# Performance work log

Measured on AMD Instinct MI355X. Metric: run time of the kernel, lower is better.

Reference implementation:

```python
import jax, jax.numpy as jnp
import numpy as np

B, NF, IN = 8, 4096, 512
NB, NW, CD = 2, 320, 384  # num_codebooks, num_codewords, codeword_dim (d_model=NB*CD=768)
TAU = 1.0


def setup_inputs() -> dict:
    key = jax.random.key(0)
    k0, k1, k2, k3, k4 = jax.random.split(key, 5)
    x = jax.random.normal(k0, (B, NF, IN), dtype=jnp.float32)
    mask = jax.random.randint(k1, (B, NF), 0, 2) == 1  # True = invalid frame
    u = jax.random.uniform(k2, (B, NF, NB, NW), jnp.float32, 1e-6, 1.0 - 1e-6)
    gumbel = -jnp.log(-jnp.log(u))
    # projection Linear(IN -> NB*NW)
    W = jax.random.normal(k3, (IN, NB * NW), jnp.float32) * np.float32(1.0 / np.sqrt(IN))
    b = jnp.zeros((NB * NW,), jnp.float32)
    # codebooks, xavier-uniform-ish init
    limit = np.float32(np.sqrt(6.0 / (NW + CD)))
    codebooks = jax.random.uniform(k4, (NB, NW, CD), jnp.float32, -limit, limit)
    return dict(x=x, W=W, b=b, codebooks=codebooks, gumbel=gumbel, mask=mask)


def reference(x, W, b, codebooks, gumbel, mask):
    Bx, NFx = x.shape[:2]
    logits = (x @ W + b).reshape(Bx, NFx, NB, NW)  # (b, nf, nb, nw)
    # hard gumbel-softmax with straight-through estimator (training path)
    y = (logits + gumbel) / TAU
    soft = jax.nn.softmax(y, axis=-1)
    hard = jax.nn.one_hot(jnp.argmax(y, axis=-1), NW, dtype=soft.dtype)
    word_probs = hard + soft - jax.lax.stop_gradient(soft)
    # diversity perplexity from plain softmax probs, masked; note: faithful to
    # source, normalization divides by mask.sum() (count of invalid frames)
    soft_probs = jax.nn.softmax(logits, axis=-1)
    valid = (~mask)[..., None, None].astype(soft_probs.dtype)
    marginal = jnp.sum(soft_probs * valid, axis=(0, 1)) / mask.sum().astype(soft_probs.dtype)
    perplexity = jnp.exp(-jnp.sum(marginal * jnp.log(marginal + 1e-7), axis=-1)).sum()
    # quantize: one-hot gather-sum over codewords, concat codebooks -> d_model
    quantized = jnp.einsum('bfnw,nwd->bfnd', word_probs, codebooks).reshape(Bx, NFx, NB * CD)
    return quantized, perplexity
```

## Files before the change

kernel.cpp:

```cpp
#include <hip/hip_runtime.h>
#include <math.h>

#define BQ   8
#define NFQ  4096
#define INQ  512
#define NBQ  2
#define NWQ  320
#define CDQ  384
#define MQ   (BQ*NFQ)
#define NTOT (NBQ*NWQ)
#define DMOD (NBQ*CDQ)
#define QOUT ((size_t)MQ*(size_t)DMOD)

#define THREADS 512
#define BM 64
#define BK 32
#define NCH (INQ/BK)
#define NMB (MQ/BM)

#define A0B 0
#define A1B 4096
#define B0B 8192
#define B1B 28672
#define SMEMB 49152
#define SSUMB 8192
#define AYMB  9216
#define AIDXB 10240
#define SCB   11264
#define IDXB  11520
#define CALB  11776

#define WT_OFF   0
#define PART_OFF 655360
#define CS_OFF   1310720
#define MC_OFF   1313280

typedef __attribute__((ext_vector_type(4))) float f32x4;
typedef __attribute__((ext_vector_type(8))) short short8;
typedef const __attribute__((address_space(1))) unsigned short gas_us;
typedef __attribute__((address_space(3))) unsigned short las_us;

static __device__ __forceinline__ unsigned f2bf(float f) {
    unsigned u = __float_as_uint(f);
    return (u + 0x7FFFu + ((u >> 16) & 1u)) >> 16;
}

static __device__ __forceinline__ uint4 pack8u(float4 a, float4 b) {
    return make_uint4(f2bf(a.x) | (f2bf(a.y) << 16),
                      f2bf(a.z) | (f2bf(a.w) << 16),
                      f2bf(b.x) | (f2bf(b.y) << 16),
                      f2bf(b.z) | (f2bf(b.w) << 16));
}

#define MCOL(M,N) \
  acc##M##N = __builtin_amdgcn_mfma_f32_16x16x32_bf16(fa##M, fb##N, acc##M##N,0,0,0);

#define STAGE_B(KC, BASE) do { \
  const unsigned short* wp_ = WtB + (KC)*BK; \
  __builtin_amdgcn_global_load_lds((gas_us*)(wp_ + gb0), (las_us*)(smem + (BASE) + lo0), 16, 0, 0); \
  __builtin_amdgcn_global_load_lds((gas_us*)(wp_ + gb1), (las_us*)(smem + (BASE) + lo1), 16, 0, 0); \
  if (tid < 256) \
    __builtin_amdgcn_global_load_lds((gas_us*)(wp_ + gb2), (las_us*)(smem + (BASE) + lo2), 16, 0, 0); \
} while(0)

#define EPI1(M,R) do { \
  const int row_ = rh*32 + M*16 + q*4 + (R); \
  const int gm_  = m0 + row_; \
  float s_ = __expf(acc##M##0[R]) + __expf(acc##M##1[R]) + __expf(acc##M##2[R]) \
           + __expf(acc##M##3[R]) + __expf(acc##M##4[R]); \
  s_ += __shfl_xor(s_,1,64); s_ += __shfl_xor(s_,2,64); \
  s_ += __shfl_xor(s_,4,64); s_ += __shfl_xor(s_,8,64); \
  const float* gp_ = gum + (size_t)gm_*NTOT + nb*NWQ + cg*80 + c15; \
  float ym_ = acc##M##0[R] + gp_[0]; int yi_ = c15; float yt_; \
  yt_ = acc##M##1[R] + gp_[16]; if (yt_>ym_){ym_=yt_; yi_=16+c15;} \
  yt_ = acc##M##2[R] + gp_[32]; if (yt_>ym_){ym_=yt_; yi_=32+c15;} \
  yt_ = acc##M##3[R] + gp_[48]; if (yt_>ym_){ym_=yt_; yi_=48+c15;} \
  yt_ = acc##M##4[R] + gp_[64]; if (yt_>ym_){ym_=yt_; yi_=64+c15;} \
  yi_ += cg*80; \
  { float ov_; int oi_; \
    ov_=__shfl_xor(ym_,1,64); oi_=__shfl_xor(yi_,1,64); if(ov_>ym_||(ov_==ym_&&oi_<yi_)){ym_=ov_;yi_=oi_;} \
    ov_=__shfl_xor(ym_,2,64); oi_=__shfl_xor(yi_,2,64); if(ov_>ym_||(ov_==ym_&&oi_<yi_)){ym_=ov_;yi_=oi_;} \
    ov_=__shfl_xor(ym_,4,64); oi_=__shfl_xor(yi_,4,64); if(ov_>ym_||(ov_==ym_&&oi_<yi_)){ym_=ov_;yi_=oi_;} \
    ov_=__shfl_xor(ym_,8,64); oi_=__shfl_xor(yi_,8,64); if(ov_>ym_||(ov_==ym_&&oi_<yi_)){ym_=ov_;yi_=oi_;} } \
  if (c15 == 0) { \
    ((float*)(smem+SSUMB))[cg*64 + row_] = s_; \
    ((float*)(smem+AYMB ))[cg*64 + row_] = ym_; \
    ((int*  )(smem+AIDXB))[cg*64 + row_] = yi_; } \
} while(0)

#define EPI2(M,R) do { \
  const int row_ = rh*32 + M*16 + q*4 + (R); \
  const float sc_ = ((float*)(smem+SCB))[row_]; \
  ca0 = fmaf(__expf(acc##M##0[R]), sc_, ca0); \
  ca1 = fmaf(__expf(acc##M##1[R]), sc_, ca1); \
  ca2 = fmaf(__expf(acc##M##2[R]), sc_, ca2); \
  ca3 = fmaf(__expf(acc##M##3[R]), sc_, ca3); \
  ca4 = fmaf(__expf(acc##M##4[R]), sc_, ca4); \
} while(0)

__global__ __launch_bounds__(256) void wcvt(const float* __restrict__ W,
                                            unsigned short* __restrict__ Wt)
{
    __shared__ __align__(16) float sm[64][68];
    const int kb = blockIdx.x, cbk = blockIdx.y;
    const int tid = threadIdx.x;
    const int r = tid >> 2, qq = tid & 3;
    const float* wp = W + (size_t)(kb*64 + r)*NTOT + cbk*64;
    *(float4*)(&sm[r][(qq   )*4]) = *(const float4*)(wp + (qq   )*4);
    *(float4*)(&sm[r][(qq+ 4)*4]) = *(const float4*)(wp + (qq+ 4)*4);
    *(float4*)(&sm[r][(qq+ 8)*4]) = *(const float4*)(wp + (qq+ 8)*4);
    *(float4*)(&sm[r][(qq+12)*4]) = *(const float4*)(wp + (qq+12)*4);
    __syncthreads();
    const int cc = tid >> 2, kq = tid & 3;
    const int k0 = kq * 16;
    const float v0=sm[k0+0][cc],  v1=sm[k0+1][cc],  v2=sm[k0+2][cc],  v3=sm[k0+3][cc],
                v4=sm[k0+4][cc],  v5=sm[k0+5][cc],  v6=sm[k0+6][cc],  v7=sm[k0+7][cc],
                v8=sm[k0+8][cc],  v9=sm[k0+9][cc],  v10=sm[k0+10][cc],v11=sm[k0+11][cc],
                v12=sm[k0+12][cc],v13=sm[k0+13][cc],v14=sm[k0+14][cc],v15=sm[k0+15][cc];
    const unsigned u0 = f2bf(v0)  | (f2bf(v1) <<16), u1 = f2bf(v2)  | (f2bf(v3) <<16),
                   u2 = f2bf(v4)  | (f2bf(v5) <<16), u3 = f2bf(v6)  | (f2bf(v7) <<16),
                   u4 = f2bf(v8)  | (f2bf(v9) <<16), u5 = f2bf(v10) | (f2bf(v11)<<16),
                   u6 = f2bf(v12) | (f2bf(v13)<<16), u7 = f2bf(v14) | (f2bf(v15)<<16);
    unsigned short* op = Wt + (size_t)(cbk*64 + cc)*INQ + kb*64 + k0;
    *(uint4*)(op)     = make_uint4(u0,u1,u2,u3);
    *(uint4*)(op + 8) = make_uint4(u4,u5,u6,u7);
}

__global__ __launch_bounds__(THREADS, 4) void qk1(
    const float* __restrict__ x, const unsigned short* __restrict__ Wt,
    const float* __restrict__ bias, const float* __restrict__ cb,
    const float* __restrict__ gum, const int* __restrict__ maskp,
    float* __restrict__ out, unsigned short* __restrict__ partial)
{
    __shared__ __align__(16) char smem[SMEMB];
    const int tid = threadIdx.x;
    const int orig = blockIdx.x;
    const int bid = ((orig & 7) << 7) | (orig >> 3);
    const int mb = bid >> 1, nb = bid & 1;
    const int m0 = mb * BM;
    const int w = tid >> 6, l = tid & 63, q = l >> 4, c15 = l & 15;
    const int cg = w & 3, rh = w >> 2;

    const int sB = tid & 3;
    const int colj0 = (tid      ) >> 2, colj1 = (tid +  512) >> 2,
              colj2 = (tid + 1024) >> 2;
    const int kgj0 = sB ^ ((colj0 >> 1) & 3), kgj1 = sB ^ ((colj1 >> 1) & 3),
              kgj2 = sB ^ ((colj2 >> 1) & 3);
    const unsigned short* WtB = Wt + (size_t)nb * NWQ * INQ;
    const int gb0 = colj0*INQ + kgj0*8, gb1 = colj1*INQ + kgj1*8,
              gb2 = colj2*INQ + kgj2*8;
    const int lo0 = (tid      )*16, lo1 = (tid+ 512)*16, lo2 = (tid+1024)*16;

    const int xt = tid & 255;
    const int xrow = xt >> 2, xh = xt & 3;
    const float* xg = x + (size_t)(m0 + xrow)*INQ + xh*8;
    const int axw = xrow*64 + ((xh ^ ((xrow >> 1) & 3)) * 16);

    const int sw = (c15 >> 1) & 3;
    const int aoff = (rh*32 + c15)*64 + ((q ^ sw) * 16);
    const int boff = (cg*80 + c15)*64 + ((q ^ sw) * 16);

    f32x4 acc00={0,0,0,0}, acc01={0,0,0,0}, acc02={0,0,0,0}, acc03={0,0,0,0}, acc04={0,0,0,0};
    f32x4 acc10={0,0,0,0}, acc11={0,0,0,0}, acc12={0,0,0,0}, acc13={0,0,0,0}, acc14={0,0,0,0};

    STAGE_B(0, B0B);
    if (tid < 256) {
        const float4 a0 = *(const float4*)(xg), a1 = *(const float4*)(xg + 4);
        *(uint4*)(smem + A0B + axw) = pack8u(a0, a1);
    }
    __syncthreads();

#pragma unroll 2
    for (int kc = 0; kc < NCH; ++kc) {
        const int p = kc & 1;
        const int Acur = p ? A1B : A0B;
        const int Anx  = p ? A0B : A1B;
        const int Bcur = p ? B1B : B0B;
        const int Bnx  = p ? B0B : B1B;
        const bool more = (kc + 1 < NCH);
        float4 n0, n1;
        if (more) {
            if (tid < 256) {
                n0 = *(const float4*)(xg + (kc+1)*BK);
                n1 = *(const float4*)(xg + (kc+1)*BK + 4);
            }
            STAGE_B(kc + 1, Bnx);
        }
        const short8 fa0 = *(const short8*)(smem + Acur + aoff);
        const short8 fa1 = *(const short8*)(smem + Acur + aoff + 1024);
        const short8 fb0 = *(const short8*)(smem + Bcur + boff);
        const short8 fb1 = *(const short8*)(smem + Bcur + boff + 1024);
        const short8 fb2 = *(const short8*)(smem + Bcur + boff + 2048);
        const short8 fb3 = *(const short8*)(smem + Bcur + boff + 3072);
        const short8 fb4 = *(const short8*)(smem + Bcur + boff + 4096);
        MCOL(0,0); MCOL(0,1); MCOL(0,2); MCOL(0,3); MCOL(0,4);
        MCOL(1,0); MCOL(1,1); MCOL(1,2); MCOL(1,3); MCOL(1,4);
        if (more && tid < 256)
            *(uint4*)(smem + Anx + axw) = pack8u(n0, n1);
        __syncthreads();
    }

    const float* bp = bias + nb*NWQ + cg*80 + c15;
    const float b0v = bp[0], b1v = bp[16], b2v = bp[32], b3v = bp[48], b4v = bp[64];
    acc00 = acc00 + b0v; acc01 = acc01 + b1v; acc02 = acc02 + b2v;
    acc03 = acc03 + b3v; acc04 = acc04 + b4v;
    acc10 = acc10 + b0v; acc11 = acc11 + b1v; acc12 = acc12 + b2v;
    acc13 = acc13 + b3v; acc14 = acc14 + b4v;

    EPI1(0,0); EPI1(0,1); EPI1(0,2); EPI1(0,3);
    EPI1(1,0); EPI1(1,1); EPI1(1,2); EPI1(1,3);
    __syncthreads();

    if (tid < BM) {
        const int row = tid;
        const float* ssum = (const float*)(smem + SSUMB);
        const float* aym  = (const float*)(smem + AYMB);
        const int*   aidx = (const int*)(smem + AIDXB);
        const float se = ssum[row] + ssum[64+row] + ssum[128+row] + ssum[192+row];
        const float vf = (maskp[m0 + row] == 0) ? 1.0f : 0.0f;
        ((float*)(smem + SCB))[row] = vf / se;
        float bv = aym[row]; int bi = aidx[row];
        float ov; int oi;
        ov = aym[ 64+row]; oi = aidx[ 64+row]; if (ov>bv || (ov==bv && oi<bi)) { bv=ov; bi=oi; }
        ov = aym[128+row]; oi = aidx[128+row]; if (ov>bv || (ov==bv && oi<bi)) { bv=ov; bi=oi; }
        ov = aym[192+row]; oi = aidx[192+row]; if (ov>bv || (ov==bv && oi<bi)) { bv=ov; bi=oi; }
        ((int*)(smem + IDXB))[row] = bi;
    }
    __syncthreads();

    float ca0=0.f, ca1=0.f, ca2=0.f, ca3=0.f, ca4=0.f;
    EPI2(0,0); EPI2(0,1); EPI2(0,2); EPI2(0,3);
    EPI2(1,0); EPI2(1,1); EPI2(1,2); EPI2(1,3);
    ca0 += __shfl_xor(ca0,16,64); ca0 += __shfl_xor(ca0,32,64);
    ca1 += __shfl_xor(ca1,16,64); ca1 += __shfl_xor(ca1,32,64);
    ca2 += __shfl_xor(ca2,16,64); ca2 += __shfl_xor(ca2,32,64);
    ca3 += __shfl_xor(ca3,16,64); ca3 += __shfl_xor(ca3,32,64);
    ca4 += __shfl_xor(ca4,16,64); ca4 += __shfl_xor(ca4,32,64);
    if (l < 16) {
        float* cal = (float*)(smem + CALB) + w*80 + c15;
        cal[0]=ca0; cal[16]=ca1; cal[32]=ca2; cal[48]=ca3; cal[64]=ca4;
    }
    __syncthreads();
    if (tid < NWQ) {
        const float* cal = (const float*)(smem + CALB);
        const float v = cal[tid] + cal[tid + 320];
        partial[(size_t)mb*NTOT + nb*NWQ + tid] = (unsigned short)f2bf(v);
    }

    const float* cbb = cb + (size_t)nb*NWQ*CDQ;
    const int* idxs = (const int*)(smem + IDXB);
    for (int t = tid; t < BM*(CDQ/4); t += THREADS) {
        const int r = t / (CDQ/4);
        const int qq = t - r*(CDQ/4);
        const int idx = idxs[r];
        float4 v = *(const float4*)(cbb + (size_t)idx*CDQ + qq*4);
        *(float4*)(out + (size_t)(m0+r)*DMOD + (size_t)nb*CDQ + qq*4) = v;
    }
}

__global__ __launch_bounds__(256) void qk2a(const unsigned short* __restrict__ partial,
                                            const int* __restrict__ maskp,
                                            float* __restrict__ colsum,
                                            int* __restrict__ maskcnt)
{
    __shared__ float fs[256];
    __shared__ int   is[4];
    const int b = blockIdx.x, tid = threadIdx.x;
    if (b < 40) {
        const int ci = tid & 15, g = tid >> 4;
        const int col = b*16 + ci;
        float s = 0.f;
        for (int r = 0; r < 32; ++r) {
            const unsigned u = partial[(size_t)(g*32 + r)*NTOT + col];
            s += __uint_as_float(u << 16);
        }
        fs[g*16 + ci] = s;
        __syncthreads();
        if (tid < 16) {
            float t = 0.f;
            for (int g2 = 0; g2 < 16; ++g2) t += fs[g2*16 + tid];
            colsum[b*16 + tid] = t;
        }
    } else {
        const int bb = b - 40;
        int ms = 0;
        for (int k2 = 0; k2 < 16; ++k2) ms += maskp[bb*4096 + tid + k2*256];
        for (int s2 = 32; s2 >= 1; s2 >>= 1) ms += __shfl_xor(ms, s2, 64);
        if ((tid & 63) == 0) is[tid >> 6] = ms;
        __syncthreads();
        if (tid == 0) maskcnt[bb] = is[0] + is[1] + is[2] + is[3];
    }
}

__global__ void qk2b(const float* __restrict__ colsum,
                     const int* __restrict__ maskcnt,
                     float* __restrict__ out)
{
    __shared__ float fred[10];
    __shared__ float s_ms;
    const int tid = threadIdx.x, lane = tid & 63, wid = tid >> 6;
    if (tid == 0) {
        int t = 0;
        for (int i = 0; i < 8; ++i) t += maskcnt[i];
        s_ms = (float)t;
    }
    __syncthreads();
    float mar = colsum[tid] / s_ms;
    float tv = mar * logf(mar + 1e-7f);
    for (int s = 32; s >= 1; s >>= 1) tv += __shfl_xor(tv, s, 64);
    if (lane == 0) fred[wid] = tv;
    __syncthreads();
    if (tid == 0) {
        float h0 = fred[0]+fred[1]+fred[2]+fred[3]+fred[4];
        float h1 = fred[5]+fred[6]+fred[7]+fred[8]+fred[9];
        out[QOUT] = expf(-h0) + expf(-h1);
    }
}

extern "C" void kernel_launch(void* const* d_in, const int* in_sizes, int n_in,
                              void* d_out, int out_size, void* d_ws, size_t ws_size,
                              hipStream_t stream) {
    const float* x    = (const float*)d_in[0];
    const float* W    = (const float*)d_in[1];
    const float* bias = (const float*)d_in[2];
    const float* cb   = (const float*)d_in[3];
    const float* gum  = (const float*)d_in[4];
    const int*   mask = (const int*)d_in[5];
    float* out = (float*)d_out;
    unsigned short* Wt      = (unsigned short*)((char*)d_ws + WT_OFF);
    unsigned short* partial = (unsigned short*)((char*)d_ws + PART_OFF);
    float*          colsum  = (float*)((char*)d_ws + CS_OFF);
    int*            maskcnt = (int*)((char*)d_ws + MC_OFF);

    wcvt<<<dim3(INQ/64, NTOT/64), 256, 0, stream>>>(W, Wt);
    qk1<<<NMB*NBQ, THREADS, 0, stream>>>(x, Wt, bias, cb, gum, mask, out, partial);
    qk2a<<<48, 256, 0, stream>>>(partial, mask, colsum, maskcnt);
    qk2b<<<1, 640, 0, stream>>>(colsum, maskcnt, out);
}
```

Baseline: 81.41 us.

## Fuse perplexity finalize into reduction kernel via last-block atomic; drop block swizzle

Merges the two final reduction kernels into one: each of the 48 blocks increments an atomic counter after a threadfence, and the last block computes the entropy and perplexity. This removes one kernel launch and its dependency gap. The counter is reset inside the weight-conversion kernel. It also removes the blockIdx remapping in the main fused kernel, which changes block scheduling order and L2 locality for the x tiles.

```diff
diff --git a/kernel.cpp b/kernel.cpp
--- a/kernel.cpp
+++ b/kernel.cpp
@@ -34,6 +34,7 @@
 #define PART_OFF 655360
 #define CS_OFF   1310720
 #define MC_OFF   1313280
+#define CNT_OFF  1313312
 
 typedef __attribute__((ext_vector_type(4))) float f32x4;
 typedef __attribute__((ext_vector_type(8))) short short8;
@@ -99,11 +100,13 @@
 } while(0)
 
 __global__ __launch_bounds__(256) void wcvt(const float* __restrict__ W,
-                                            unsigned short* __restrict__ Wt)
+                                            unsigned short* __restrict__ Wt,
+                                            int* __restrict__ cnt)
 {
     __shared__ __align__(16) float sm[64][68];
     const int kb = blockIdx.x, cbk = blockIdx.y;
     const int tid = threadIdx.x;
+    if (kb == 0 && cbk == 0 && tid == 0) *cnt = 0;
     const int r = tid >> 2, qq = tid & 3;
     const float* wp = W + (size_t)(kb*64 + r)*NTOT + cbk*64;
     *(float4*)(&sm[r][(qq   )*4]) = *(const float4*)(wp + (qq   )*4);
@@ -134,8 +137,7 @@
 {
     __shared__ __align__(16) char smem[SMEMB];
     const int tid = threadIdx.x;
-    const int orig = blockIdx.x;
-    const int bid = ((orig & 7) << 7) | (orig >> 3);
+    const int bid = blockIdx.x;
     const int mb = bid >> 1, nb = bid & 1;
     const int m0 = mb * BM;
     const int w = tid >> 6, l = tid & 63, q = l >> 4, c15 = l & 15;
@@ -258,13 +260,16 @@
     }
 }
 
-__global__ __launch_bounds__(256) void qk2a(const unsigned short* __restrict__ partial,
-                                            const int* __restrict__ maskp,
-                                            float* __restrict__ colsum,
-                                            int* __restrict__ maskcnt)
+__global__ __launch_bounds__(256) void qk2(const unsigned short* __restrict__ partial,
+                                           const int* __restrict__ maskp,
+                                           float* __restrict__ colsum,
+                                           int* __restrict__ maskcnt,
+                                           int* __restrict__ cnt,
+                                           float* __restrict__ out)
 {
     __shared__ float fs[256];
     __shared__ int   is[4];
+    __shared__ int   lastf;
     const int b = blockIdx.x, tid = threadIdx.x;
     if (b < 40) {
         const int ci = tid & 15, g = tid >> 4;
@@ -290,30 +295,39 @@
         __syncthreads();
         if (tid == 0) maskcnt[bb] = is[0] + is[1] + is[2] + is[3];
     }
-}
-
-__global__ void qk2b(const float* __restrict__ colsum,
-                     const int* __restrict__ maskcnt,
-                     float* __restrict__ out)
-{
-    __shared__ float fred[10];
-    __shared__ float s_ms;
-    const int tid = threadIdx.x, lane = tid & 63, wid = tid >> 6;
+    __threadfence();
+    if (tid == 0) {
+        const int old = atomicAdd(cnt, 1);
+        lastf = (old == 47);
+    }
+    __syncthreads();
+    if (!lastf) return;
+    __threadfence();
+
     if (tid == 0) {
         int t = 0;
         for (int i = 0; i < 8; ++i) t += maskcnt[i];
-        s_ms = (float)t;
-    }
-    __syncthreads();
-    float mar = colsum[tid] / s_ms;
-    float tv = mar * logf(mar + 1e-7f);
-    for (int s = 32; s >= 1; s >>= 1) tv += __shfl_xor(tv, s, 64);
-    if (lane == 0) fred[wid] = tv;
+        fs[0] = (float)t;
+    }
+    __syncthreads();
+    const float sm_f = fs[0];
+    float h0 = 0.f, h1 = 0.f;
+    for (int c = tid; c < NTOT; c += 256) {
+        const float mar = colsum[c] / sm_f;
+        const float tv = mar * logf(mar + 1e-7f);
+        if (c < NWQ) h0 += tv; else h1 += tv;
+    }
+    for (int s2 = 32; s2 >= 1; s2 >>= 1) {
+        h0 += __shfl_xor(h0, s2, 64);
+        h1 += __shfl_xor(h1, s2, 64);
+    }
+    __syncthreads();
+    if ((tid & 63) == 0) { fs[tid >> 6] = h0; fs[4 + (tid >> 6)] = h1; }
     __syncthreads();
     if (tid == 0) {
-        float h0 = fred[0]+fred[1]+fred[2]+fred[3]+fred[4];
-        float h1 = fred[5]+fred[6]+fred[7]+fred[8]+fred[9];
-        out[QOUT] = expf(-h0) + expf(-h1);
+        const float H0 = fs[0]+fs[1]+fs[2]+fs[3];
+        const float H1 = fs[4]+fs[5]+fs[6]+fs[7];
+        out[QOUT] = expf(-H0) + expf(-H1);
     }
 }
 
@@ -331,9 +345,9 @@
     unsigned short* partial = (unsigned short*)((char*)d_ws + PART_OFF);
     float*          colsum  = (float*)((char*)d_ws + CS_OFF);
     int*            maskcnt = (int*)((char*)d_ws + MC_OFF);
-
-    wcvt<<<dim3(INQ/64, NTOT/64), 256, 0, stream>>>(W, Wt);
+    int*            cnt     = (int*)((char*)d_ws + CNT_OFF);
+
+    wcvt<<<dim3(INQ/64, NTOT/64), 256, 0, stream>>>(W, Wt, cnt);
     qk1<<<NMB*NBQ, THREADS, 0, stream>>>(x, Wt, bias, cb, gum, mask, out, partial);
-    qk2a<<<48, 256, 0, stream>>>(partial, mask, colsum, maskcnt);
-    qk2b<<<1, 640, 0, stream>>>(colsum, maskcnt, out);
-}
+    qk2<<<48, 256, 0, stream>>>(partial, mask, colsum, maskcnt, cnt, out);
+}
```

Result: no change. 80.80 us (-0.7%).
